# Kernel optimization log

Measured on AMD Instinct MI355X. Metric: run time of the kernel, lower is better.

The kernel has to match this reference:

```python
import jax, jax.numpy as jnp
import numpy as np

N_GENE, N_CT, N_REF, N_SAMPLE = 50000, 64, 16, 1024

def setup_inputs() -> dict:
    key = jax.random.key(0)
    k1, k2, k3, k4, k5, k6 = jax.random.split(key, 6)
    x = jax.random.normal(k1, (N_GENE * N_CT * N_REF,), dtype=jnp.float32)
    idx = jax.random.randint(k2, (N_CT, N_GENE), 0, N_CT * N_GENE)
    # RefCombLayer weight: uniform around 1/n_ref
    num = 1.0 / N_REF
    w_ref = jax.random.uniform(k3, (N_REF * N_CT,), minval=num - num / 5, maxval=num + num / 5, dtype=jnp.float32)
    # CelltypeScaleLayer weight: normal(1.0, 0.1)
    w_ct = 1.0 + 0.1 * jax.random.normal(k4, (N_CT,), dtype=jnp.float32)
    # StretchLayer weight: normal(1.0, 0.1)
    w_stretch = 1.0 + 0.1 * jax.random.normal(k5, (N_GENE,), dtype=jnp.float32)
    # conv1 kernel: (n_sample, 1, n_kernel), normal(1/n_ct, 0.25/n_ct)
    conv_w = (1.0 / N_CT) + (0.25 / N_CT) * jax.random.normal(k6, (N_SAMPLE, 1, N_CT), dtype=jnp.float32)
    return {"x": x, "idx": idx, "w_ref": w_ref, "w_ct": w_ct,
            "w_stretch": w_stretch, "conv_w": conv_w,
            "N_batch": 1, "N_feature": N_GENE * N_CT}


def reference(x, idx, w_ref, w_ct, w_stretch, conv_w, N_batch, N_feature):
    # RefCombLayer: elementwise mul by per-gene-tiled ref weights
    y = x * jnp.tile(w_ref, N_GENE)                       # [n_gene*n_ct*n_ref]
    # SliceSumLayer: sum over n_ref slices
    y0 = y.reshape(N_CT * N_GENE, N_REF).sum(axis=1)      # [n_ct*n_gene]
    # CelltypeScaleLayer: gather per cell type, scale, flatten transposed
    z = y0[idx] * w_ct[:, None]                           # [n_ct, n_gene]
    y1 = z.T.reshape(-1)                                  # [n_gene*n_ct], gene-major
    # StretchLayer: per-gene weight repeated n_ct times
    y2 = y1 * jnp.repeat(w_stretch, N_CT)                 # [n_gene*n_ct]
    # Conv1d(1, n_sample, kernel=n_ct, stride=n_ct) == per-gene dot with kernel
    yk = y2.reshape(N_GENE, N_CT)                         # [n_gene, n_ct]
    out = jnp.einsum('gk,sk->sg', yk, conv_w[:, 0, :])    # [n_sample, n_gene]
    return (out, y0, y1, y2)
```

## Files before the change

### kernel.cpp

```cpp
#include <hip/hip_runtime.h>
#include <hip/hip_fp16.h>

#define NG 50000
#define NCT 64
#define NREF 16
#define NS 1024
#define N0 (NCT * NG)

#define OFF_Y0 ((size_t)NS * NG)
#define OFF_Y1 (OFF_Y0 + N0)
#define OFF_Y2 (OFF_Y1 + N0)

typedef __attribute__((ext_vector_type(8))) short bf16x8;
typedef __attribute__((ext_vector_type(4))) float f32x4;

__device__ __forceinline__ unsigned short f2bf(float f) {
    union { float f; unsigned u; } v; v.f = f;
    unsigned r = v.u + 0x7fff + ((v.u >> 16) & 1);
    return (unsigned short)(r >> 16);
}
__device__ __forceinline__ float bf2f(unsigned short b) {
    union { float f; unsigned u; } v; v.u = ((unsigned)b) << 16;
    return v.f;
}

template<bool H16>
__global__ __launch_bounds__(256) void k_y0(const float* __restrict__ x,
                                            const float* __restrict__ w_ref,
                                            float* __restrict__ y0,
                                            __half* __restrict__ y0h) {
    __shared__ f32x4 wl[256];
    const int tid = threadIdx.x;
    wl[tid] = reinterpret_cast<const f32x4*>(w_ref)[tid];
    __syncthreads();
    const int row = tid & 63;
    const f32x4 w0 = wl[row * 4 + 0];
    const f32x4 w1 = wl[row * 4 + 1];
    const f32x4 w2 = wl[row * 4 + 2];
    const f32x4 w3 = wl[row * 4 + 3];
    const f32x4* x4 = reinterpret_cast<const f32x4*>(x);
    const size_t stride = (size_t)gridDim.x * 256;
    for (size_t j = (size_t)blockIdx.x * 256 + tid; j < (size_t)N0; j += stride) {
        const f32x4* xp = x4 + j * 4;
        f32x4 a = __builtin_nontemporal_load(xp + 0);
        f32x4 b = __builtin_nontemporal_load(xp + 1);
        f32x4 c = __builtin_nontemporal_load(xp + 2);
        f32x4 d = __builtin_nontemporal_load(xp + 3);
        float s = a.x * w0.x + a.y * w0.y + a.z * w0.z + a.w * w0.w
                + b.x * w1.x + b.y * w1.y + b.z * w1.z + b.w * w1.w
                + c.x * w2.x + c.y * w2.y + c.z * w2.z + c.w * w2.w
                + d.x * w3.x + d.y * w3.y + d.z * w3.z + d.w * w3.w;
        y0[j] = s;
        if (H16) y0h[j] = __float2half(s);
    }
}

template<bool H16>
__global__ __launch_bounds__(512) void k_pc(const float* __restrict__ y0,
                                            const __half* __restrict__ y0h,
                                            const int* __restrict__ idx,
                                            const float* __restrict__ w_ct,
                                            const float* __restrict__ w_stretch,
                                            const float* __restrict__ cw,
                                            float* __restrict__ y1,
                                            float* __restrict__ y2,
                                            float* __restrict__ out) {
    __shared__ float T[4][64 * 9];
    __shared__ unsigned short Phi[2][32 * 72];
    __shared__ unsigned short Plo[2][32 * 72];

    const int tid  = threadIdx.x;
    const int lane = tid & 63;
    const int wid  = tid >> 6;
    const int g0   = blockIdx.x * 64;

    if (wid < 4) {
        const int p = wid;
        const float wct = w_ct[lane];
        float* Tp = T[p];

        int iids[16];
#pragma unroll
        for (int h = 0; h < 2; ++h)
#pragma unroll
            for (int k = 0; k < 8; ++k) {
                int j = lane & 7;
                int c = (lane >> 3) + k * 8;
                int g = min(g0 + 32 * h + p * 8 + j, NG - 1);
                iids[h * 8 + k] = __builtin_nontemporal_load(idx + c * NG + g);
            }
        float vals[16];
#pragma unroll
        for (int k = 0; k < 16; ++k) {
            if (H16) vals[k] = __half2float(y0h[iids[k]]);
            else     vals[k] = y0[iids[k]];
        }

        for (int h = 0; h < 2; ++h) {
            const int gbase = g0 + 32 * h + p * 8;
#pragma unroll
            for (int k = 0; k < 8; ++k) {
                int j = lane & 7;
                int c = (lane >> 3) + k * 8;
                Tp[c * 9 + j] = vals[h * 8 + k];
            }
#pragma unroll
            for (int j = 0; j < 8; ++j) {
                int g = gbase + j;
                float t = Tp[lane * 9 + j];
                float v1 = t * wct;
                float v2 = v1 * w_stretch[min(g, NG - 1)];
                int base = (p * 8 + j) * 72 + lane;
                unsigned short hh = f2bf(v2);
                Phi[h][base] = hh;
                Plo[h][base] = f2bf(v2 - bf2f(hh));
                if (g < NG) {
                    size_t o = (size_t)g * 64 + lane;
                    __builtin_nontemporal_store(v1, y1 + o);
                    __builtin_nontemporal_store(v2, y2 + o);
                }
            }
            __syncthreads();
        }
    } else {
        const int cwv = wid - 4;
        const int l15 = lane & 15;
        const int l4  = lane >> 4;
        __syncthreads();
        for (int h = 0; h < 2; ++h) {
            bf16x8 Ah[2][2], Al[2][2];
#pragma unroll
            for (int m = 0; m < 2; ++m) {
                int grow = m * 16 + l15;
#pragma unroll
                for (int ks = 0; ks < 2; ++ks) {
                    int koff = ks * 32 + l4 * 8;
                    Ah[m][ks] = *reinterpret_cast<const bf16x8*>(&Phi[h][grow * 72 + koff]);
                    Al[m][ks] = *reinterpret_cast<const bf16x8*>(&Plo[h][grow * 72 + koff]);
                }
            }
            const int gh = g0 + 32 * h;
            for (int s0 = 0; s0 < NS; s0 += 128) {
                f32x4 acc[2][2];
#pragma unroll
                for (int m = 0; m < 2; ++m)
#pragma unroll
                    for (int n = 0; n < 2; ++n) acc[m][n] = (f32x4){0.f, 0.f, 0.f, 0.f};
#pragma unroll
                for (int n = 0; n < 2; ++n) {
                    const size_t srow = (size_t)(s0 + cwv * 32 + n * 16 + l15) * 64;
                    bf16x8 Bh[2], Bl[2];
#pragma unroll
                    for (int ks = 0; ks < 2; ++ks) {
                        int koff = ks * 32 + l4 * 8;
                        f32x4 va = *reinterpret_cast<const f32x4*>(cw + srow + koff);
                        f32x4 vb = *reinterpret_cast<const f32x4*>(cw + srow + koff + 4);
#pragma unroll
                        for (int e = 0; e < 4; ++e) {
                            unsigned short hv = f2bf(va[e]);
                            Bh[ks][e] = (short)hv;
                            Bl[ks][e] = (short)f2bf(va[e] - bf2f(hv));
                            hv = f2bf(vb[e]);
                            Bh[ks][e + 4] = (short)hv;
                            Bl[ks][e + 4] = (short)f2bf(vb[e] - bf2f(hv));
                        }
                    }
#pragma unroll
                    for (int m = 0; m < 2; ++m)
#pragma unroll
                        for (int ks = 0; ks < 2; ++ks) {
                            acc[m][n] = __builtin_amdgcn_mfma_f32_16x16x32_bf16(Ah[m][ks], Bh[ks], acc[m][n], 0, 0, 0);
                            acc[m][n] = __builtin_amdgcn_mfma_f32_16x16x32_bf16(Ah[m][ks], Bl[ks], acc[m][n], 0, 0, 0);
                            acc[m][n] = __builtin_amdgcn_mfma_f32_16x16x32_bf16(Al[m][ks], Bh[ks], acc[m][n], 0, 0, 0);
                        }
                }
#pragma unroll
                for (int m = 0; m < 2; ++m) {
                    int g4 = gh + m * 16 + l4 * 4;
                    if (g4 < NG) {
#pragma unroll
                        for (int n = 0; n < 2; ++n) {
                            int s = s0 + cwv * 32 + n * 16 + l15;
                            __builtin_nontemporal_store(acc[m][n], reinterpret_cast<f32x4*>(out + (size_t)s * NG + g4));
                        }
                    }
                }
            }
            if (h == 0) __syncthreads();
        }
    }
}

extern "C" void kernel_launch(void* const* d_in, const int* in_sizes, int n_in,
                              void* d_out, int out_size, void* d_ws, size_t ws_size,
                              hipStream_t stream) {
    const float* x         = (const float*)d_in[0];
    const int*   idx       = (const int*)d_in[1];
    const float* w_ref     = (const float*)d_in[2];
    const float* w_ct      = (const float*)d_in[3];
    const float* w_stretch = (const float*)d_in[4];
    const float* conv_w    = (const float*)d_in[5];

    float* out = (float*)d_out;
    float* y0  = out + OFF_Y0;
    float* y1  = out + OFF_Y1;
    float* y2  = out + OFF_Y2;

    const bool h16 = (ws_size >= (size_t)N0 * sizeof(__half));
    __half* y0h = (__half*)d_ws;

    if (h16) {
        k_y0<true><<<2048, 256, 0, stream>>>(x, w_ref, y0, y0h);
        k_pc<true><<<(NG + 63) / 64, 512, 0, stream>>>(y0, y0h, idx, w_ct, w_stretch,
                                                       conv_w, y1, y2, out);
    } else {
        k_y0<false><<<2048, 256, 0, stream>>>(x, w_ref, y0, nullptr);
        k_pc<false><<<(NG + 63) / 64, 512, 0, stream>>>(y0, nullptr, idx, w_ct, w_stretch,
                                                        conv_w, y1, y2, out);
    }
}
```

Before: 175.2 us.

## Make gather/MFMA kernel persistent with double-buffered producer-consumer tiles

Turns the second kernel into a persistent kernel with 256 blocks, each looping over 64-gene tiles. Four producer waves gather and scale tile i into one LDS buffer while four MFMA waves compute the conv output for tile i-1 from the other buffer. The goal is to overlap the latency-bound gather with the write-heavy GEMM output and to cut block launch overhead. The MFMA waves now handle 64 genes per tile instead of two 32-gene halves. With only 256 blocks, occupancy is lower, and each iteration adds a block-wide barrier.

```diff
diff --git a/kernel.cpp b/kernel.cpp
--- a/kernel.cpp
+++ b/kernel.cpp
@@ -6,6 +6,8 @@
 #define NREF 16
 #define NS 1024
 #define N0 (NCT * NG)
+#define NTILES 782
+#define NB 256
 
 #define OFF_Y0 ((size_t)NS * NG)
 #define OFF_Y1 (OFF_Y0 + N0)
@@ -56,68 +58,76 @@
 }
 
 template<bool H16>
-__global__ __launch_bounds__(512) void k_pc(const float* __restrict__ y0,
-                                            const __half* __restrict__ y0h,
-                                            const int* __restrict__ idx,
-                                            const float* __restrict__ w_ct,
-                                            const float* __restrict__ w_stretch,
-                                            const float* __restrict__ cw,
-                                            float* __restrict__ y1,
-                                            float* __restrict__ y2,
-                                            float* __restrict__ out) {
+__global__ __launch_bounds__(512) void k_pipe(const float* __restrict__ y0,
+                                              const __half* __restrict__ y0h,
+                                              const int* __restrict__ idx,
+                                              const float* __restrict__ w_ct,
+                                              const float* __restrict__ w_stretch,
+                                              const float* __restrict__ cw,
+                                              float* __restrict__ y1,
+                                              float* __restrict__ y2,
+                                              float* __restrict__ out) {
     __shared__ float T[4][64 * 9];
-    __shared__ unsigned short Phi[2][32 * 72];
-    __shared__ unsigned short Plo[2][32 * 72];
+    __shared__ unsigned short Phi[2][64 * 72];
+    __shared__ unsigned short Plo[2][64 * 72];
 
     const int tid  = threadIdx.x;
     const int lane = tid & 63;
     const int wid  = tid >> 6;
-    const int g0   = blockIdx.x * 64;
+
+    int ntiles = 0;
+    for (int t = blockIdx.x; t < NTILES; t += NB) ++ntiles;
 
     if (wid < 4) {
         const int p = wid;
         const float wct = w_ct[lane];
         float* Tp = T[p];
-
-        int iids[16];
-#pragma unroll
-        for (int h = 0; h < 2; ++h)
-#pragma unroll
-            for (int k = 0; k < 8; ++k) {
-                int j = lane & 7;
-                int c = (lane >> 3) + k * 8;
-                int g = min(g0 + 32 * h + p * 8 + j, NG - 1);
-                iids[h * 8 + k] = __builtin_nontemporal_load(idx + c * NG + g);
-            }
-        float vals[16];
-#pragma unroll
-        for (int k = 0; k < 16; ++k) {
-            if (H16) vals[k] = __half2float(y0h[iids[k]]);
-            else     vals[k] = y0[iids[k]];
-        }
-
-        for (int h = 0; h < 2; ++h) {
-            const int gbase = g0 + 32 * h + p * 8;
-#pragma unroll
-            for (int k = 0; k < 8; ++k) {
-                int j = lane & 7;
-                int c = (lane >> 3) + k * 8;
-                Tp[c * 9 + j] = vals[h * 8 + k];
-            }
-#pragma unroll
-            for (int j = 0; j < 8; ++j) {
-                int g = gbase + j;
-                float t = Tp[lane * 9 + j];
-                float v1 = t * wct;
-                float v2 = v1 * w_stretch[min(g, NG - 1)];
-                int base = (p * 8 + j) * 72 + lane;
-                unsigned short hh = f2bf(v2);
-                Phi[h][base] = hh;
-                Plo[h][base] = f2bf(v2 - bf2f(hh));
-                if (g < NG) {
-                    size_t o = (size_t)g * 64 + lane;
-                    __builtin_nontemporal_store(v1, y1 + o);
-                    __builtin_nontemporal_store(v2, y2 + o);
+        for (int it = 0; it <= ntiles; ++it) {
+            if (it < ntiles) {
+                const int tile = blockIdx.x + it * NB;
+                const int g0   = tile * 64;
+                const int buf  = it & 1;
+                int iids[16];
+#pragma unroll
+                for (int grp = 0; grp < 2; ++grp)
+#pragma unroll
+                    for (int k = 0; k < 8; ++k) {
+                        int j = lane & 7;
+                        int c = (lane >> 3) + k * 8;
+                        int g = min(g0 + p * 16 + grp * 8 + j, NG - 1);
+                        iids[grp * 8 + k] = __builtin_nontemporal_load(idx + c * NG + g);
+                    }
+                float vals[16];
+#pragma unroll
+                for (int k = 0; k < 16; ++k) {
+                    if (H16) vals[k] = __half2float(y0h[iids[k]]);
+                    else     vals[k] = y0[iids[k]];
+                }
+#pragma unroll
+                for (int grp = 0; grp < 2; ++grp) {
+                    const int gbase = g0 + p * 16 + grp * 8;
+#pragma unroll
+                    for (int k = 0; k < 8; ++k) {
+                        int j = lane & 7;
+                        int c = (lane >> 3) + k * 8;
+                        Tp[c * 9 + j] = vals[grp * 8 + k];
+                    }
+#pragma unroll
+                    for (int j = 0; j < 8; ++j) {
+                        int g = gbase + j;
+                        float t = Tp[lane * 9 + j];
+                        float v1 = t * wct;
+                        float v2 = v1 * w_stretch[min(g, NG - 1)];
+                        int r = p * 16 + grp * 8 + j;
+                        unsigned short hh = f2bf(v2);
+                        Phi[buf][r * 72 + lane] = hh;
+                        Plo[buf][r * 72 + lane] = f2bf(v2 - bf2f(hh));
+                        if (g < NG) {
+                            size_t o = (size_t)g * 64 + lane;
+                            __builtin_nontemporal_store(v1, y1 + o);
+                            __builtin_nontemporal_store(v2, y2 + o);
+                        }
+                    }
                 }
             }
             __syncthreads();
@@ -126,67 +136,70 @@
         const int cwv = wid - 4;
         const int l15 = lane & 15;
         const int l4  = lane >> 4;
-        __syncthreads();
-        for (int h = 0; h < 2; ++h) {
-            bf16x8 Ah[2][2], Al[2][2];
-#pragma unroll
-            for (int m = 0; m < 2; ++m) {
-                int grow = m * 16 + l15;
-#pragma unroll
-                for (int ks = 0; ks < 2; ++ks) {
-                    int koff = ks * 32 + l4 * 8;
-                    Ah[m][ks] = *reinterpret_cast<const bf16x8*>(&Phi[h][grow * 72 + koff]);
-                    Al[m][ks] = *reinterpret_cast<const bf16x8*>(&Plo[h][grow * 72 + koff]);
-                }
-            }
-            const int gh = g0 + 32 * h;
-            for (int s0 = 0; s0 < NS; s0 += 128) {
-                f32x4 acc[2][2];
-#pragma unroll
-                for (int m = 0; m < 2; ++m)
-#pragma unroll
-                    for (int n = 0; n < 2; ++n) acc[m][n] = (f32x4){0.f, 0.f, 0.f, 0.f};
-#pragma unroll
-                for (int n = 0; n < 2; ++n) {
-                    const size_t srow = (size_t)(s0 + cwv * 32 + n * 16 + l15) * 64;
-                    bf16x8 Bh[2], Bl[2];
+        for (int it = 0; it <= ntiles; ++it) {
+            if (it >= 1) {
+                const int tile = blockIdx.x + (it - 1) * NB;
+                const int g0   = tile * 64;
+                const int buf  = (it - 1) & 1;
+                bf16x8 Ah[4][2], Al[4][2];
+#pragma unroll
+                for (int m = 0; m < 4; ++m) {
+                    int grow = m * 16 + l15;
 #pragma unroll
                     for (int ks = 0; ks < 2; ++ks) {
                         int koff = ks * 32 + l4 * 8;
-                        f32x4 va = *reinterpret_cast<const f32x4*>(cw + srow + koff);
-                        f32x4 vb = *reinterpret_cast<const f32x4*>(cw + srow + koff + 4);
-#pragma unroll
-                        for (int e = 0; e < 4; ++e) {
-                            unsigned short hv = f2bf(va[e]);
-                            Bh[ks][e] = (short)hv;
-                            Bl[ks][e] = (short)f2bf(va[e] - bf2f(hv));
-                            hv = f2bf(vb[e]);
-                            Bh[ks][e + 4] = (short)hv;
-                            Bl[ks][e + 4] = (short)f2bf(vb[e] - bf2f(hv));
+                        Ah[m][ks] = *reinterpret_cast<const bf16x8*>(&Phi[buf][grow * 72 + koff]);
+                        Al[m][ks] = *reinterpret_cast<const bf16x8*>(&Plo[buf][grow * 72 + koff]);
+                    }
+                }
+                for (int s0 = 0; s0 < NS; s0 += 128) {
+                    f32x4 acc[4][2];
+#pragma unroll
+                    for (int m = 0; m < 4; ++m)
+#pragma unroll
+                        for (int n = 0; n < 2; ++n) acc[m][n] = (f32x4){0.f, 0.f, 0.f, 0.f};
+#pragma unroll
+                    for (int n = 0; n < 2; ++n) {
+                        const size_t srow = (size_t)(s0 + cwv * 32 + n * 16 + l15) * 64;
+                        bf16x8 Bh[2], Bl[2];
+#pragma unroll
+                        for (int ks = 0; ks < 2; ++ks) {
+                            int koff = ks * 32 + l4 * 8;
+                            f32x4 va = *reinterpret_cast<const f32x4*>(cw + srow + koff);
+                            f32x4 vb = *reinterpret_cast<const f32x4*>(cw + srow + koff + 4);
+#pragma unroll
+                            for (int e = 0; e < 4; ++e) {
+                                unsigned short hv = f2bf(va[e]);
+                                Bh[ks][e] = (short)hv;
+                                Bl[ks][e] = (short)f2bf(va[e] - bf2f(hv));
+                                hv = f2bf(vb[e]);
+                                Bh[ks][e + 4] = (short)hv;
+                                Bl[ks][e + 4] = (short)f2bf(vb[e] - bf2f(hv));
+                            }
                         }
-                    }
-#pragma unroll
-                    for (int m = 0; m < 2; ++m)
-#pragma unroll
-                        for (int ks = 0; ks < 2; ++ks) {
-                            acc[m][n] = __builtin_amdgcn_mfma_f32_16x16x32_bf16(Ah[m][ks], Bh[ks], acc[m][n], 0, 0, 0);
-                            acc[m][n] = __builtin_amdgcn_mfma_f32_16x16x32_bf16(Ah[m][ks], Bl[ks], acc[m][n], 0, 0, 0);
-                            acc[m][n] = __builtin_amdgcn_mfma_f32_16x16x32_bf16(Al[m][ks], Bh[ks], acc[m][n], 0, 0, 0);
+#pragma unroll
+                        for (int m = 0; m < 4; ++m)
+#pragma unroll
+                            for (int ks = 0; ks < 2; ++ks) {
+                                acc[m][n] = __builtin_amdgcn_mfma_f32_16x16x32_bf16(Ah[m][ks], Bh[ks], acc[m][n], 0, 0, 0);
+                                acc[m][n] = __builtin_amdgcn_mfma_f32_16x16x32_bf16(Ah[m][ks], Bl[ks], acc[m][n], 0, 0, 0);
+                                acc[m][n] = __builtin_amdgcn_mfma_f32_16x16x32_bf16(Al[m][ks], Bh[ks], acc[m][n], 0, 0, 0);
+                            }
+                    }
+#pragma unroll
+                    for (int m = 0; m < 4; ++m) {
+                        int g4 = g0 + m * 16 + l4 * 4;
+                        if (g4 < NG) {
+#pragma unroll
+                            for (int n = 0; n < 2; ++n) {
+                                int s = s0 + cwv * 32 + n * 16 + l15;
+                                __builtin_nontemporal_store(acc[m][n], reinterpret_cast<f32x4*>(out + (size_t)s * NG + g4));
+                            }
                         }
-                }
-#pragma unroll
-                for (int m = 0; m < 2; ++m) {
-                    int g4 = gh + m * 16 + l4 * 4;
-                    if (g4 < NG) {
-#pragma unroll
-                        for (int n = 0; n < 2; ++n) {
-                            int s = s0 + cwv * 32 + n * 16 + l15;
-                            __builtin_nontemporal_store(acc[m][n], reinterpret_cast<f32x4*>(out + (size_t)s * NG + g4));
-                        }
                     }
                 }
             }
-            if (h == 0) __syncthreads();
+            __syncthreads();
         }
     }
 }
@@ -211,11 +224,11 @@
 
     if (h16) {
         k_y0<true><<<2048, 256, 0, stream>>>(x, w_ref, y0, y0h);
-        k_pc<true><<<(NG + 63) / 64, 512, 0, stream>>>(y0, y0h, idx, w_ct, w_stretch,
-                                                       conv_w, y1, y2, out);
+        k_pipe<true><<<NB, 512, 0, stream>>>(y0, y0h, idx, w_ct, w_stretch,
+                                             conv_w, y1, y2, out);
     } else {
         k_y0<false><<<2048, 256, 0, stream>>>(x, w_ref, y0, nullptr);
-        k_pc<false><<<(NG + 63) / 64, 512, 0, stream>>>(y0, nullptr, idx, w_ct, w_stretch,
-                                                        conv_w, y1, y2, out);
+        k_pipe<false><<<NB, 512, 0, stream>>>(y0, nullptr, idx, w_ct, w_stretch,
+                                              conv_w, y1, y2, out);
     }
 }
```

New measurement: 177.1 us. No clear change (+1.0%).
